# Kernel tuning notes

Hardware: AMD Instinct MI355X
Metric: run time of the kernel (lower is better)

Reference implementation:

```python
import jax, jax.numpy as jnp
import numpy as np

# Mamba hyperparams derived from DRMamba.__init__: d_model=dim=96, d_state=16, d_conv=4, expand=2
D_MODEL = 96
D_INNER = 192          # expand * d_model
D_STATE = 16
D_CONV = 4
DT_RANK = 6            # ceil(d_model / 16)
REVERSE = True


def setup_inputs() -> dict:
    key = jax.random.key(0)
    ks = jax.random.split(key, 8)
    s = lambda k, shape: jax.random.normal(k, shape, jnp.float32) * 0.02
    x = jax.random.normal(ks[0], (8, 96, 64, 64), jnp.float32)
    in_proj_w = s(ks[1], (2 * D_INNER, D_MODEL))
    conv_w = s(ks[2], (D_INNER, 1, D_CONV))            # depthwise conv kernel (O, I/groups=1, K)
    conv_b = jnp.zeros((D_INNER,), jnp.float32)
    x_proj_w = s(ks[3], (DT_RANK + 2 * D_STATE, D_INNER))
    dt_proj_w = s(ks[4], (D_INNER, DT_RANK))
    dt_proj_b = s(ks[5], (D_INNER,))
    # S4D-real init, as in standard Mamba
    A_log = jnp.log(jnp.broadcast_to(jnp.arange(1, D_STATE + 1, dtype=jnp.float32), (D_INNER, D_STATE)))
    D = jnp.ones((D_INNER,), jnp.float32)
    out_proj_w = s(ks[6], (D_MODEL, D_INNER))
    return dict(x=x, in_proj_w=in_proj_w, conv_w=conv_w, conv_b=conv_b,
                x_proj_w=x_proj_w, dt_proj_w=dt_proj_w, dt_proj_b=dt_proj_b,
                A_log=A_log, D=D, out_proj_w=out_proj_w)


def reference(x, in_proj_w, conv_w, conv_b, x_proj_w, dt_proj_w, dt_proj_b, A_log, D, out_proj_w):
    b, c, h, w = x.shape
    xs = jnp.flip(x, 1) if REVERSE else x
    seq = xs.reshape(b, c, h * w).transpose(0, 2, 1)              # (b, l, d_model)
    xz = seq @ in_proj_w.T                                        # (b, l, 2*d_inner)
    u, res = jnp.split(xz, 2, axis=-1)
    # causal depthwise conv1d over sequence (torch: padding=d_conv-1 then truncate to l)
    uc = jax.lax.conv_general_dilated(
        u.transpose(0, 2, 1), conv_w, (1,), [(D_CONV - 1, 0)],
        dimension_numbers=('NCH', 'OIH', 'NCH'), feature_group_count=D_INNER)
    uc = uc + conv_b[None, :, None]
    u = jax.nn.silu(uc.transpose(0, 2, 1))                        # (b, l, d_inner)
    # input-dependent SSM parameters
    dbc = u @ x_proj_w.T                                          # (b, l, dt_rank + 2*d_state)
    dt, B, C = jnp.split(dbc, [DT_RANK, DT_RANK + D_STATE], axis=-1)
    delta = jax.nn.softplus(dt @ dt_proj_w.T + dt_proj_b)         # (b, l, d_inner)
    A = -jnp.exp(A_log)                                           # (d_inner, d_state)
    dA = jnp.exp(jnp.einsum('bld,dn->bldn', delta, A))            # discretized A
    dBu = jnp.einsum('bld,bln,bld->bldn', delta, B, u)            # discretized B * u

    def step(state, inp):
        dA_t, dBu_t, C_t = inp                                    # (b,d,n), (b,d,n), (b,n)
        state = dA_t * state + dBu_t
        y_t = jnp.einsum('bdn,bn->bd', state, C_t)
        return state, y_t

    init = jnp.zeros((b, D_INNER, D_STATE), u.dtype)
    _, ys = jax.lax.scan(step, init,
                         (dA.transpose(1, 0, 2, 3), dBu.transpose(1, 0, 2, 3), C.transpose(1, 0, 2)))
    y = ys.transpose(1, 0, 2) + u * D                             # (b, l, d_inner)
    y = y * jax.nn.silu(res)
    out = y @ out_proj_w.T                                        # (b, l, d_model)
    out = out.transpose(0, 2, 1).reshape(b, c, h, w)
    return jnp.flip(out, 1) if REVERSE else out
```

## Files before the change

### kernel.cpp

```cpp
#include <hip/hip_runtime.h>
#include <math.h>

#define NBATCH 8
#define SEQL   4096
#define DMODEL 96
#define DINNER 192
#define DSTATE 16
#define NDBC   38
#define NCHUNK 128
#define CSTEP  32

__device__ __forceinline__ float siluf(float x) {
    return x / (1.f + expf(-x));
}
__device__ __forceinline__ float softplusf(float x) {
    return (x > 20.f) ? x : log1pf(expf(x));
}

__global__ __launch_bounds__(256) void k_in_proj(const float* __restrict__ x,
                                                 const float* __restrict__ w,
                                                 float* __restrict__ u_raw,
                                                 float* __restrict__ res)
{
    __shared__ float As[32][128];
    __shared__ float Ws[64][33];
    const int tid = threadIdx.x;
    const int tx = tid & 15, ty = tid >> 4;
    const int b = blockIdx.z;
    const int l0 = blockIdx.x * 128;
    const int jb = blockIdx.y * 64;

    float acc[8][4];
#pragma unroll
    for (int r = 0; r < 8; r++)
#pragma unroll
        for (int c = 0; c < 4; c++) acc[r][c] = 0.f;

    for (int kb = 0; kb < 3; kb++) {
        {
            const int ll4 = tid & 31;
            const int mb = tid >> 5;
#pragma unroll
            for (int i = 0; i < 4; i++) {
                const int m = mb + 8 * i;
                const float4 v = *reinterpret_cast<const float4*>(
                    &x[((size_t)b * 96 + (95 - (kb * 32 + m))) * 4096 + l0 + ll4 * 4]);
                *reinterpret_cast<float4*>(&As[m][ll4 * 4]) = v;
            }
        }
        {
            const int k4 = tid & 7;
            const int jb0 = tid >> 3;
#pragma unroll
            for (int i = 0; i < 2; i++) {
                const int jl = jb0 + 32 * i;
                const float4 v = *reinterpret_cast<const float4*>(
                    &w[(size_t)(jb + jl) * 96 + kb * 32 + k4 * 4]);
                Ws[jl][k4 * 4 + 0] = v.x;
                Ws[jl][k4 * 4 + 1] = v.y;
                Ws[jl][k4 * 4 + 2] = v.z;
                Ws[jl][k4 * 4 + 3] = v.w;
            }
        }
        __syncthreads();
#pragma unroll
        for (int k = 0; k < 32; k++) {
            const float4 a0 = *reinterpret_cast<const float4*>(&As[k][ty * 8]);
            const float4 a1 = *reinterpret_cast<const float4*>(&As[k][ty * 8 + 4]);
            const float av[8] = {a0.x, a0.y, a0.z, a0.w, a1.x, a1.y, a1.z, a1.w};
            float wv[4];
#pragma unroll
            for (int c = 0; c < 4; c++) wv[c] = Ws[tx * 4 + c][k];
#pragma unroll
            for (int r = 0; r < 8; r++)
#pragma unroll
                for (int c = 0; c < 4; c++) acc[r][c] = fmaf(av[r], wv[c], acc[r][c]);
        }
        __syncthreads();
    }

    float* outp;
    int col0;
    if (jb < 192) { outp = u_raw; col0 = jb + tx * 4; }
    else          { outp = res;   col0 = jb - 192 + tx * 4; }
#pragma unroll
    for (int r = 0; r < 8; r++) {
        const int row = l0 + ty * 8 + r;
        const float4 v = make_float4(acc[r][0], acc[r][1], acc[r][2], acc[r][3]);
        *reinterpret_cast<float4*>(&outp[((size_t)b * 4096 + row) * 192 + col0]) = v;
    }
}

__global__ __launch_bounds__(192) void k_conv(const float* __restrict__ u_raw,
                                              const float* __restrict__ cw,
                                              const float* __restrict__ cb,
                                              float* __restrict__ u)
{
    const int d = threadIdx.x;
    const int t0 = blockIdx.x * 4;
    const int b = blockIdx.y;
    const float4 w4 = *reinterpret_cast<const float4*>(&cw[d * 4]);
    const float bias = cb[d];
    float v[7];
#pragma unroll
    for (int i = 0; i < 7; i++) {
        const int tt = t0 - 3 + i;
        v[i] = (tt >= 0) ? u_raw[((size_t)b * 4096 + tt) * 192 + d] : 0.f;
    }
#pragma unroll
    for (int j = 0; j < 4; j++) {
        float s = bias;
        s = fmaf(w4.x, v[j + 0], s);
        s = fmaf(w4.y, v[j + 1], s);
        s = fmaf(w4.z, v[j + 2], s);
        s = fmaf(w4.w, v[j + 3], s);
        u[((size_t)b * 4096 + t0 + j) * 192 + d] = siluf(s);
    }
}

__global__ __launch_bounds__(256) void k_xproj(const float* __restrict__ u,
                                               const float* __restrict__ w,
                                               float* __restrict__ dbc,
                                               float* __restrict__ Barr,
                                               float* __restrict__ Carr)
{
    __shared__ float Ws[64 * 32];
    const int tid = threadIdx.x, tx = tid & 15, ty = tid >> 4;
    const int b = blockIdx.z;
    const int l0 = blockIdx.x * 128;

    float acc[8][4];
#pragma unroll
    for (int r = 0; r < 8; r++)
#pragma unroll
        for (int c = 0; c < 4; c++) acc[r][c] = 0.f;

    for (int kb = 0; kb < 6; kb++) {
        {
            const int k4 = tid & 7;
            const int jb0 = tid >> 3;
#pragma unroll
            for (int i = 0; i < 2; i++) {
                const int jl = jb0 + 32 * i;
                float4 v = make_float4(0.f, 0.f, 0.f, 0.f);
                if (jl < NDBC)
                    v = *reinterpret_cast<const float4*>(&w[(size_t)jl * 192 + kb * 32 + k4 * 4]);
                *reinterpret_cast<float4*>(
                    &Ws[jl * 32 + ((k4 ^ ((jl >> 2) & 7)) << 2)]) = v;
            }
        }
        __syncthreads();
        const int sw = tx & 7;
#pragma unroll
        for (int k4 = 0; k4 < 8; k4++) {
            float4 a4[8];
#pragma unroll
            for (int r = 0; r < 8; r++) {
                const int row = l0 + ty * 8 + r;
                a4[r] = *reinterpret_cast<const float4*>(
                    &u[((size_t)b * 4096 + row) * 192 + kb * 32 + k4 * 4]);
            }
            float4 w4[4];
#pragma unroll
            for (int c = 0; c < 4; c++)
                w4[c] = *reinterpret_cast<const float4*>(
                    &Ws[(tx * 4 + c) * 32 + ((k4 ^ sw) << 2)]);
#pragma unroll
            for (int r = 0; r < 8; r++)
#pragma unroll
                for (int c = 0; c < 4; c++) {
                    acc[r][c] = fmaf(a4[r].x, w4[c].x, acc[r][c]);
                    acc[r][c] = fmaf(a4[r].y, w4[c].y, acc[r][c]);
                    acc[r][c] = fmaf(a4[r].z, w4[c].z, acc[r][c]);
                    acc[r][c] = fmaf(a4[r].w, w4[c].w, acc[r][c]);
                }
        }
        __syncthreads();
    }
#pragma unroll
    for (int r = 0; r < 8; r++) {
        const size_t row = (size_t)blockIdx.z * 4096 + l0 + ty * 8 + r;
#pragma unroll
        for (int c = 0; c < 4; c++) {
            const int j = tx * 4 + c;
            if (j < 6)       dbc[row * NDBC + j] = acc[r][c];
            else if (j < 22) Barr[row * 16 + (j - 6)] = acc[r][c];
            else if (j < 38) Carr[row * 16 + (j - 22)] = acc[r][c];
        }
    }
}

__global__ __launch_bounds__(768) void k_dtproj(const float* __restrict__ dbc,
                                                const float* __restrict__ w,
                                                const float* __restrict__ bias,
                                                float* __restrict__ delta)
{
    const int j = threadIdx.x;
    const int row = blockIdx.x * 4 + threadIdx.y;
    const int b = blockIdx.y;
    const size_t g = (size_t)b * 4096 + row;
    const float* dr = &dbc[g * NDBC];
    float s = bias[j];
#pragma unroll
    for (int k = 0; k < 6; k++) s = fmaf(dr[k], w[j * 6 + k], s);
    delta[g * 192 + j] = softplusf(s);
}

__global__ __launch_bounds__(192) void k_scan1(const float* __restrict__ delta,
                                               const float* __restrict__ u,
                                               const float* __restrict__ Barr,
                                               const float* __restrict__ A_log,
                                               float* __restrict__ P,
                                               float* __restrict__ S)
{
    const int d = threadIdx.x;
    const int c = blockIdx.x;
    const int b = blockIdx.y;

    float a[16];
    {
        const float4* al = reinterpret_cast<const float4*>(&A_log[d * 16]);
#pragma unroll
        for (int i = 0; i < 4; i++) {
            const float4 v = al[i];
            a[4 * i + 0] = -expf(v.x);
            a[4 * i + 1] = -expf(v.y);
            a[4 * i + 2] = -expf(v.z);
            a[4 * i + 3] = -expf(v.w);
        }
    }
    float st[16], p[16];
#pragma unroll
    for (int n = 0; n < 16; n++) { st[n] = 0.f; p[n] = 1.f; }

    const size_t g0 = (size_t)b * 4096 + (size_t)c * CSTEP;
    const float* dp = delta + g0 * 192 + d;
    const float* up = u + g0 * 192 + d;
    const float* bp = Barr + g0 * 16;

#pragma unroll 2
    for (int t = 0; t < CSTEP; t++) {
        const float dt = dp[t * 192];
        const float dtu = dt * up[t * 192];
        float Bv[16];
        {
            const float4* b4 = reinterpret_cast<const float4*>(bp + t * 16);
#pragma unroll
            for (int i = 0; i < 4; i++) {
                const float4 v = b4[i];
                Bv[4 * i + 0] = v.x; Bv[4 * i + 1] = v.y;
                Bv[4 * i + 2] = v.z; Bv[4 * i + 3] = v.w;
            }
        }
#pragma unroll
        for (int n = 0; n < 16; n++) {
            const float dA = __expf(dt * a[n]);
            p[n] *= dA;
            st[n] = fmaf(dA, st[n], dtu * Bv[n]);
        }
    }

    const size_t idx = (((size_t)b * NCHUNK + c) * 192 + d) * 16;
    float4* Pp = reinterpret_cast<float4*>(&P[idx]);
    float4* Sp = reinterpret_cast<float4*>(&S[idx]);
#pragma unroll
    for (int i = 0; i < 4; i++) {
        Pp[i] = make_float4(p[4 * i], p[4 * i + 1], p[4 * i + 2], p[4 * i + 3]);
        Sp[i] = make_float4(st[4 * i], st[4 * i + 1], st[4 * i + 2], st[4 * i + 3]);
    }
}

__global__ __launch_bounds__(256) void k_scan2(const float* __restrict__ P,
                                               float* __restrict__ S)
{
    const int dn = blockIdx.x * 256 + threadIdx.x;
    const int b = blockIdx.y;
    float carry = 0.f;
    const size_t base = (size_t)b * NCHUNK * 3072 + dn;
#pragma unroll 8
    for (int c = 0; c < NCHUNK; c++) {
        const size_t idx = base + (size_t)c * 3072;
        const float p = P[idx];
        const float s = S[idx];
        S[idx] = carry;
        carry = fmaf(p, carry, s);
    }
}

__global__ __launch_bounds__(192) void k_scan3(const float* __restrict__ delta,
                                               const float* __restrict__ u,
                                               const float* __restrict__ Barr,
                                               const float* __restrict__ Carr,
                                               const float* __restrict__ A_log,
                                               const float* __restrict__ S,
                                               const float* __restrict__ Dp,
                                               const float* __restrict__ res,
                                               float* __restrict__ y)
{
    const int d = threadIdx.x;
    const int c = blockIdx.x;
    const int b = blockIdx.y;

    float a[16];
    {
        const float4* al = reinterpret_cast<const float4*>(&A_log[d * 16]);
#pragma unroll
        for (int i = 0; i < 4; i++) {
            const float4 v = al[i];
            a[4 * i + 0] = -expf(v.x);
            a[4 * i + 1] = -expf(v.y);
            a[4 * i + 2] = -expf(v.z);
            a[4 * i + 3] = -expf(v.w);
        }
    }
    float st[16];
    {
        const float4* Sp = reinterpret_cast<const float4*>(
            &S[(((size_t)b * NCHUNK + c) * 192 + d) * 16]);
#pragma unroll
        for (int i = 0; i < 4; i++) {
            const float4 v = Sp[i];
            st[4 * i + 0] = v.x; st[4 * i + 1] = v.y;
            st[4 * i + 2] = v.z; st[4 * i + 3] = v.w;
        }
    }
    const float Dd = Dp[d];

    const size_t g0 = (size_t)b * 4096 + (size_t)c * CSTEP;
    const float* dp = delta + g0 * 192 + d;
    const float* up = u + g0 * 192 + d;
    const float* rp = res + g0 * 192 + d;
    float* yp = y + g0 * 192 + d;
    const float* bp = Barr + g0 * 16;
    const float* cp = Carr + g0 * 16;

#pragma unroll 2
    for (int t = 0; t < CSTEP; t++) {
        const float dt = dp[t * 192];
        const float ut = up[t * 192];
        const float dtu = dt * ut;
        float Bv[16], Cv[16];
        {
            const float4* b4 = reinterpret_cast<const float4*>(bp + t * 16);
            const float4* c4 = reinterpret_cast<const float4*>(cp + t * 16);
#pragma unroll
            for (int i = 0; i < 4; i++) {
                const float4 v = b4[i];
                Bv[4 * i + 0] = v.x; Bv[4 * i + 1] = v.y;
                Bv[4 * i + 2] = v.z; Bv[4 * i + 3] = v.w;
                const float4 w = c4[i];
                Cv[4 * i + 0] = w.x; Cv[4 * i + 1] = w.y;
                Cv[4 * i + 2] = w.z; Cv[4 * i + 3] = w.w;
            }
        }
        float yt = 0.f;
#pragma unroll
        for (int n = 0; n < 16; n++) {
            const float dA = __expf(dt * a[n]);
            st[n] = fmaf(dA, st[n], dtu * Bv[n]);
            yt = fmaf(st[n], Cv[n], yt);
        }
        const float r = rp[t * 192];
        const float sig = __builtin_amdgcn_rcpf(1.f + __expf(-r));
        yp[t * 192] = fmaf(ut, Dd, yt) * (r * sig);
    }
}

__global__ __launch_bounds__(256) void k_outproj(const float* __restrict__ y,
                                                 const float* __restrict__ w,
                                                 float* __restrict__ out)
{
    __shared__ float Ws[64 * 32];
    const int tid = threadIdx.x, tx = tid & 15, ty = tid >> 4;
    const int b = blockIdx.z;
    const int l0 = blockIdx.x * 128;
    const int jb = blockIdx.y * 64;

    float acc[8][4];
#pragma unroll
    for (int r = 0; r < 8; r++)
#pragma unroll
        for (int c = 0; c < 4; c++) acc[r][c] = 0.f;

    for (int kb = 0; kb < 6; kb++) {
        {
            const int k4 = tid & 7;
            const int jb0 = tid >> 3;
#pragma unroll
            for (int i = 0; i < 2; i++) {
                const int jl = jb0 + 32 * i;
                const int j = jb + jl;
                float4 v = make_float4(0.f, 0.f, 0.f, 0.f);
                if (j < 96)
                    v = *reinterpret_cast<const float4*>(&w[(size_t)j * 192 + kb * 32 + k4 * 4]);
                *reinterpret_cast<float4*>(
                    &Ws[jl * 32 + ((k4 ^ ((jl >> 2) & 7)) << 2)]) = v;
            }
        }
        __syncthreads();
        const int sw = tx & 7;
#pragma unroll
        for (int k4 = 0; k4 < 8; k4++) {
            float4 a4[8];
#pragma unroll
            for (int r = 0; r < 8; r++) {
                const int row = l0 + ty * 8 + r;
                a4[r] = *reinterpret_cast<const float4*>(
                    &y[((size_t)b * 4096 + row) * 192 + kb * 32 + k4 * 4]);
            }
            float4 w4[4];
#pragma unroll
            for (int c = 0; c < 4; c++)
                w4[c] = *reinterpret_cast<const float4*>(
                    &Ws[(tx * 4 + c) * 32 + ((k4 ^ sw) << 2)]);
#pragma unroll
            for (int r = 0; r < 8; r++)
#pragma unroll
                for (int c = 0; c < 4; c++) {
                    acc[r][c] = fmaf(a4[r].x, w4[c].x, acc[r][c]);
                    acc[r][c] = fmaf(a4[r].y, w4[c].y, acc[r][c]);
                    acc[r][c] = fmaf(a4[r].z, w4[c].z, acc[r][c]);
                    acc[r][c] = fmaf(a4[r].w, w4[c].w, acc[r][c]);
                }
        }
        __syncthreads();
    }
#pragma unroll
    for (int c = 0; c < 4; c++) {
        const int j = jb + tx * 4 + c;
        if (j < 96) {
            const int ch = 95 - j;
            const float4 v0 = make_float4(acc[0][c], acc[1][c], acc[2][c], acc[3][c]);
            const float4 v1 = make_float4(acc[4][c], acc[5][c], acc[6][c], acc[7][c]);
            const size_t base = ((size_t)b * 96 + ch) * 4096 + l0 + ty * 8;
            *reinterpret_cast<float4*>(&out[base]) = v0;
            *reinterpret_cast<float4*>(&out[base + 4]) = v1;
        }
    }
}

extern "C" void kernel_launch(void* const* d_in, const int* in_sizes, int n_in,
                              void* d_out, int out_size, void* d_ws, size_t ws_size,
                              hipStream_t stream)
{
    const float* x       = (const float*)d_in[0];
    const float* in_w    = (const float*)d_in[1];
    const float* conv_w  = (const float*)d_in[2];
    const float* conv_b  = (const float*)d_in[3];
    const float* xproj_w = (const float*)d_in[4];
    const float* dt_w    = (const float*)d_in[5];
    const float* dt_b    = (const float*)d_in[6];
    const float* A_log   = (const float*)d_in[7];
    const float* Dp      = (const float*)d_in[8];
    const float* out_w   = (const float*)d_in[9];

    float* ws    = (float*)d_ws;
    float* u_raw = ws;
    float* res   = u_raw + 6291456;
    float* u     = res   + 6291456;
    float* delta = u     + 6291456;
    float* dbc   = delta + 6291456;
    float* Barr  = dbc   + 1245184;
    float* Carr  = Barr  + 524288;
    float* P     = Carr  + 524288;
    float* S     = P     + 3145728;
    float* yfin  = u_raw;

    hipLaunchKernelGGL(k_in_proj, dim3(32, 6, 8), dim3(256), 0, stream, x, in_w, u_raw, res);
    hipLaunchKernelGGL(k_conv,    dim3(1024, 8),  dim3(192), 0, stream, u_raw, conv_w, conv_b, u);
    hipLaunchKernelGGL(k_xproj,   dim3(32, 1, 8), dim3(256), 0, stream, u, xproj_w, dbc, Barr, Carr);
    hipLaunchKernelGGL(k_dtproj,  dim3(1024, 8),  dim3(192, 4), 0, stream, dbc, dt_w, dt_b, delta);
    hipLaunchKernelGGL(k_scan1,   dim3(NCHUNK, 8), dim3(192), 0, stream, delta, u, Barr, A_log, P, S);
    hipLaunchKernelGGL(k_scan2,   dim3(12, 8),    dim3(256), 0, stream, P, S);
    hipLaunchKernelGGL(k_scan3,   dim3(NCHUNK, 8), dim3(192), 0, stream, delta, u, Barr, Carr, A_log, S, Dp, res, yfin);
    hipLaunchKernelGGL(k_outproj, dim3(32, 2, 8), dim3(256), 0, stream, yfin, out_w, (float*)d_out);
}
```

Baseline: 280.4 us.

## Fuse causal conv+SiLU into x_proj kernel and retile in_proj to 8x8 per thread

The separate depthwise conv kernel is removed. The x_proj kernel now loads u_raw tiles with a 3-row halo into shared memory, computes conv+SiLU there, writes u out for the later scan, and feeds the GEMM from shared memory instead of global. This removes one launch and a full read of u. in_proj switches to 128 threads, each with an 8x8 output tile and a transposed weight tile that allows vectorized LDS reads. The trade-off is fewer threads per block and more registers in in_proj, plus extra syncs and a halo reload in x_proj.

```diff
diff --git a/kernel.cpp b/kernel.cpp
--- a/kernel.cpp
+++ b/kernel.cpp
@@ -17,32 +17,33 @@
     return (x > 20.f) ? x : log1pf(expf(x));
 }
 
-__global__ __launch_bounds__(256) void k_in_proj(const float* __restrict__ x,
+__global__ __launch_bounds__(128) void k_in_proj(const float* __restrict__ x,
                                                  const float* __restrict__ w,
                                                  float* __restrict__ u_raw,
                                                  float* __restrict__ res)
 {
     __shared__ float As[32][128];
-    __shared__ float Ws[64][33];
+    __shared__ float Wt[32][68];
     const int tid = threadIdx.x;
-    const int tx = tid & 15, ty = tid >> 4;
+    const int jg = tid & 7;
+    const int lg = tid >> 3;
     const int b = blockIdx.z;
     const int l0 = blockIdx.x * 128;
     const int jb = blockIdx.y * 64;
 
-    float acc[8][4];
+    float acc[8][8];
 #pragma unroll
     for (int r = 0; r < 8; r++)
 #pragma unroll
-        for (int c = 0; c < 4; c++) acc[r][c] = 0.f;
+        for (int c = 0; c < 8; c++) acc[r][c] = 0.f;
 
     for (int kb = 0; kb < 3; kb++) {
         {
             const int ll4 = tid & 31;
-            const int mb = tid >> 5;
-#pragma unroll
-            for (int i = 0; i < 4; i++) {
-                const int m = mb + 8 * i;
+            const int m0 = tid >> 5;
+#pragma unroll
+            for (int i = 0; i < 8; i++) {
+                const int m = m0 + 4 * i;
                 const float4 v = *reinterpret_cast<const float4*>(
                     &x[((size_t)b * 96 + (95 - (kb * 32 + m))) * 4096 + l0 + ll4 * 4]);
                 *reinterpret_cast<float4*>(&As[m][ll4 * 4]) = v;
@@ -50,92 +51,89 @@
         }
         {
             const int k4 = tid & 7;
-            const int jb0 = tid >> 3;
-#pragma unroll
-            for (int i = 0; i < 2; i++) {
-                const int jl = jb0 + 32 * i;
+            const int jl0 = tid >> 3;
+#pragma unroll
+            for (int i = 0; i < 4; i++) {
+                const int jl = jl0 + 16 * i;
                 const float4 v = *reinterpret_cast<const float4*>(
                     &w[(size_t)(jb + jl) * 96 + kb * 32 + k4 * 4]);
-                Ws[jl][k4 * 4 + 0] = v.x;
-                Ws[jl][k4 * 4 + 1] = v.y;
-                Ws[jl][k4 * 4 + 2] = v.z;
-                Ws[jl][k4 * 4 + 3] = v.w;
+                Wt[k4 * 4 + 0][jl] = v.x;
+                Wt[k4 * 4 + 1][jl] = v.y;
+                Wt[k4 * 4 + 2][jl] = v.z;
+                Wt[k4 * 4 + 3][jl] = v.w;
             }
         }
         __syncthreads();
 #pragma unroll
         for (int k = 0; k < 32; k++) {
-            const float4 a0 = *reinterpret_cast<const float4*>(&As[k][ty * 8]);
-            const float4 a1 = *reinterpret_cast<const float4*>(&As[k][ty * 8 + 4]);
+            const float4 a0 = *reinterpret_cast<const float4*>(&As[k][lg * 8]);
+            const float4 a1 = *reinterpret_cast<const float4*>(&As[k][lg * 8 + 4]);
+            const float4 w0 = *reinterpret_cast<const float4*>(&Wt[k][jg * 8]);
+            const float4 w1 = *reinterpret_cast<const float4*>(&Wt[k][jg * 8 + 4]);
             const float av[8] = {a0.x, a0.y, a0.z, a0.w, a1.x, a1.y, a1.z, a1.w};
-            float wv[4];
-#pragma unroll
-            for (int c = 0; c < 4; c++) wv[c] = Ws[tx * 4 + c][k];
+            const float wv[8] = {w0.x, w0.y, w0.z, w0.w, w1.x, w1.y, w1.z, w1.w};
 #pragma unroll
             for (int r = 0; r < 8; r++)
 #pragma unroll
-                for (int c = 0; c < 4; c++) acc[r][c] = fmaf(av[r], wv[c], acc[r][c]);
+                for (int c = 0; c < 8; c++) acc[r][c] = fmaf(av[r], wv[c], acc[r][c]);
         }
         __syncthreads();
     }
 
     float* outp;
     int col0;
-    if (jb < 192) { outp = u_raw; col0 = jb + tx * 4; }
-    else          { outp = res;   col0 = jb - 192 + tx * 4; }
+    if (jb < 192) { outp = u_raw; col0 = jb + jg * 8; }
+    else          { outp = res;   col0 = jb - 192 + jg * 8; }
 #pragma unroll
     for (int r = 0; r < 8; r++) {
-        const int row = l0 + ty * 8 + r;
-        const float4 v = make_float4(acc[r][0], acc[r][1], acc[r][2], acc[r][3]);
-        *reinterpret_cast<float4*>(&outp[((size_t)b * 4096 + row) * 192 + col0]) = v;
-    }
-}
-
-__global__ __launch_bounds__(192) void k_conv(const float* __restrict__ u_raw,
-                                              const float* __restrict__ cw,
-                                              const float* __restrict__ cb,
-                                              float* __restrict__ u)
-{
-    const int d = threadIdx.x;
-    const int t0 = blockIdx.x * 4;
-    const int b = blockIdx.y;
-    const float4 w4 = *reinterpret_cast<const float4*>(&cw[d * 4]);
-    const float bias = cb[d];
-    float v[7];
-#pragma unroll
-    for (int i = 0; i < 7; i++) {
-        const int tt = t0 - 3 + i;
-        v[i] = (tt >= 0) ? u_raw[((size_t)b * 4096 + tt) * 192 + d] : 0.f;
-    }
-#pragma unroll
-    for (int j = 0; j < 4; j++) {
-        float s = bias;
-        s = fmaf(w4.x, v[j + 0], s);
-        s = fmaf(w4.y, v[j + 1], s);
-        s = fmaf(w4.z, v[j + 2], s);
-        s = fmaf(w4.w, v[j + 3], s);
-        u[((size_t)b * 4096 + t0 + j) * 192 + d] = siluf(s);
-    }
-}
-
-__global__ __launch_bounds__(256) void k_xproj(const float* __restrict__ u,
+        const int row = l0 + lg * 8 + r;
+        float* rowp = &outp[((size_t)b * 4096 + row) * 192 + col0];
+        *reinterpret_cast<float4*>(rowp) =
+            make_float4(acc[r][0], acc[r][1], acc[r][2], acc[r][3]);
+        *reinterpret_cast<float4*>(rowp + 4) =
+            make_float4(acc[r][4], acc[r][5], acc[r][6], acc[r][7]);
+    }
+}
+
+__global__ __launch_bounds__(256) void k_xproj(const float* __restrict__ u_raw,
                                                const float* __restrict__ w,
+                                               const float* __restrict__ cw,
+                                               const float* __restrict__ cb,
+                                               float* __restrict__ u,
                                                float* __restrict__ dbc,
                                                float* __restrict__ Barr,
                                                float* __restrict__ Carr)
 {
+    __shared__ float Ur[67][33];
+    __shared__ float Us[64][36];
     __shared__ float Ws[64 * 32];
     const int tid = threadIdx.x, tx = tid & 15, ty = tid >> 4;
-    const int b = blockIdx.z;
-    const int l0 = blockIdx.x * 128;
-
-    float acc[8][4];
-#pragma unroll
-    for (int r = 0; r < 8; r++)
+    const int b = blockIdx.y;
+    const int l0 = blockIdx.x * 64;
+
+    float acc[4][4];
+#pragma unroll
+    for (int r = 0; r < 4; r++)
 #pragma unroll
         for (int c = 0; c < 4; c++) acc[r][c] = 0.f;
 
+    const int ch = tid & 31;
+    const int lblk = tid >> 5;
+
     for (int kb = 0; kb < 6; kb++) {
+        for (int idx = tid; idx < 536; idx += 256) {
+            const int row = idx >> 3;
+            const int c4 = idx & 7;
+            const int gl = l0 - 3 + row;
+            float4 v = make_float4(0.f, 0.f, 0.f, 0.f);
+            if (gl >= 0)
+                v = *reinterpret_cast<const float4*>(
+                    &u_raw[((size_t)b * 4096 + gl) * 192 + kb * 32 + c4 * 4]);
+            Ur[row][c4 * 4 + 0] = v.x;
+            Ur[row][c4 * 4 + 1] = v.y;
+            Ur[row][c4 * 4 + 2] = v.z;
+            Ur[row][c4 * 4 + 3] = v.w;
+        }
         {
             const int k4 = tid & 7;
             const int jb0 = tid >> 3;
@@ -150,23 +148,45 @@
             }
         }
         __syncthreads();
+
+        {
+            const float4 wc = *reinterpret_cast<const float4*>(&cw[(kb * 32 + ch) * 4]);
+            const float bias = cb[kb * 32 + ch];
+#pragma unroll
+            for (int r = 0; r < 8; r++) {
+                const int l = lblk * 8 + r;
+                float s = bias;
+                s = fmaf(wc.x, Ur[l + 0][ch], s);
+                s = fmaf(wc.y, Ur[l + 1][ch], s);
+                s = fmaf(wc.z, Ur[l + 2][ch], s);
+                s = fmaf(wc.w, Ur[l + 3][ch], s);
+                Us[l][ch] = siluf(s);
+            }
+        }
+        __syncthreads();
+
+        for (int idx = tid; idx < 512; idx += 256) {
+            const int row = idx >> 3;
+            const int c4 = idx & 7;
+            const float4 v = *reinterpret_cast<const float4*>(&Us[row][c4 * 4]);
+            *reinterpret_cast<float4*>(
+                &u[((size_t)b * 4096 + l0 + row) * 192 + kb * 32 + c4 * 4]) = v;
+        }
+
         const int sw = tx & 7;
 #pragma unroll
         for (int k4 = 0; k4 < 8; k4++) {
-            float4 a4[8];
-#pragma unroll
-            for (int r = 0; r < 8; r++) {
-                const int row = l0 + ty * 8 + r;
-                a4[r] = *reinterpret_cast<const float4*>(
-                    &u[((size_t)b * 4096 + row) * 192 + kb * 32 + k4 * 4]);
-            }
+            float4 a4[4];
+#pragma unroll
+            for (int r = 0; r < 4; r++)
+                a4[r] = *reinterpret_cast<const float4*>(&Us[ty * 4 + r][k4 * 4]);
             float4 w4[4];
 #pragma unroll
             for (int c = 0; c < 4; c++)
                 w4[c] = *reinterpret_cast<const float4*>(
                     &Ws[(tx * 4 + c) * 32 + ((k4 ^ sw) << 2)]);
 #pragma unroll
-            for (int r = 0; r < 8; r++)
+            for (int r = 0; r < 4; r++)
 #pragma unroll
                 for (int c = 0; c < 4; c++) {
                     acc[r][c] = fmaf(a4[r].x, w4[c].x, acc[r][c]);
@@ -177,9 +197,10 @@
         }
         __syncthreads();
     }
-#pragma unroll
-    for (int r = 0; r < 8; r++) {
-        const size_t row = (size_t)blockIdx.z * 4096 + l0 + ty * 8 + r;
+
+#pragma unroll
+    for (int r = 0; r < 4; r++) {
+        const size_t row = (size_t)b * 4096 + l0 + ty * 4 + r;
 #pragma unroll
         for (int c = 0; c < 4; c++) {
             const int j = tx * 4 + c;
@@ -466,9 +487,9 @@
     float* S     = P     + 3145728;
     float* yfin  = u_raw;
 
-    hipLaunchKernelGGL(k_in_proj, dim3(32, 6, 8), dim3(256), 0, stream, x, in_w, u_raw, res);
-    hipLaunchKernelGGL(k_conv,    dim3(1024, 8),  dim3(192), 0, stream, u_raw, conv_w, conv_b, u);
-    hipLaunchKernelGGL(k_xproj,   dim3(32, 1, 8), dim3(256), 0, stream, u, xproj_w, dbc, Barr, Carr);
+    hipLaunchKernelGGL(k_in_proj, dim3(32, 6, 8), dim3(128), 0, stream, x, in_w, u_raw, res);
+    hipLaunchKernelGGL(k_xproj,   dim3(64, 8),    dim3(256), 0, stream,
+                       u_raw, xproj_w, conv_w, conv_b, u, dbc, Barr, Carr);
     hipLaunchKernelGGL(k_dtproj,  dim3(1024, 8),  dim3(192, 4), 0, stream, dbc, dt_w, dt_b, delta);
     hipLaunchKernelGGL(k_scan1,   dim3(NCHUNK, 8), dim3(192), 0, stream, delta, u, Barr, A_log, P, S);
     hipLaunchKernelGGL(k_scan2,   dim3(12, 8),    dim3(256), 0, stream, P, S);
```

Result: no change. 280.0 us (-0.2%).
